# Kernel optimization log

Measured on AMD Instinct MI355X. Metric: run time of the kernel, lower is better.

Reference implementation:

```python
import jax, jax.numpy as jnp
import numpy as np

VOXEL_DIM = 16
CELL_DIM = 1.0
AA, A = 21, 14  # 20 amino acids + 'X'; atom14 representation
X_LBL = AA - 1  # label used for unknown residues


def make_voxel():
    v = VOXEL_DIM
    ax = jnp.arange(v, dtype=jnp.float32)
    vx = jnp.broadcast_to((ax - v / 2).reshape(-1, 1, 1), (v, v, v))
    vy = jnp.broadcast_to((ax - v / 4).reshape(1, -1, 1), (v, v, v))
    vz = jnp.broadcast_to((ax - v / 2).reshape(1, 1, -1), (v, v, v))
    return CELL_DIM * jnp.stack([vx, vy, vz], axis=3)  # (Vx,Vy,Vz,3)


def setup_inputs() -> dict:
    key = jax.random.key(0)
    k1, k2, k3, k4 = jax.random.split(key, 4)
    ZN = 1024
    C = 3.0 * jax.random.normal(k1, (ZN, A, 3), dtype=jnp.float32)
    L = jax.random.randint(k2, (ZN,), 0, AA)
    atom_mask = jnp.ones((ZN, A), dtype=jnp.float32)
    charges = 0.5 * jax.random.normal(k3, (AA, A), dtype=jnp.float32)
    return {"C": C, "L": L, "atom_mask": atom_mask, "charges": charges}


def get_backbone(C):
    n, ca, c = C[:, 0, :], C[:, 1, :], C[:, 2, :]
    b1 = ca - n
    b2 = c - ca
    b3 = jnp.cross(b1, b2)
    cb = ca - 0.58273431 * b2 + 0.56802827 * b1 - 0.54067466 * b3
    return jnp.stack([n, ca, c, cb], axis=1)  # (ZN,4,3)


def compute_frames(Cb):
    y = Cb[:, 3, :] - Cb[:, 1, :]
    y_unit = y / jnp.clip(jnp.linalg.norm(y, axis=1, keepdims=True), 1e-6)
    x_raw = Cb[:, 2, :] - Cb[:, 0, :]
    x_proj = jnp.sum(x_raw * y_unit, axis=1, keepdims=True)
    x = x_raw - x_proj
    x_unit = x / jnp.clip(jnp.linalg.norm(x, axis=1, keepdims=True), 1e-6)
    z = jnp.cross(x_unit, y_unit)
    z_unit = z / jnp.clip(jnp.linalg.norm(z, axis=1, keepdims=True), 1e-6)
    frames = jnp.stack([x_unit, y_unit, z_unit], axis=1)  # (ZN,3,3)
    return Cb[:, 3, :], frames


def compute_voxels(origins, frames, voxel):
    # rotation[n,x,y,z,s] = sum_u frames[n,u,s] * voxel[x,y,z,u]
    rot = jnp.einsum('nus,xyzu->nxyzs', frames, voxel)
    return origins[:, None, None, None, :] + rot  # (ZN,Vx,Vy,Vz,3)


def compute_fields(C, L, voxels, atom_mask, charges):
    L = jnp.where(L == -1, X_LBL, L)
    # (ZN,Vx,Vy,Vz,A,3)
    dv = voxels[:, :, :, :, None, :] - C[:, None, None, None, :, :]
    d = jnp.linalg.norm(dv, axis=-1, keepdims=True)
    dist_term = dv / (jnp.where(d == 0, 1.0, d) * jnp.clip(d, CELL_DIM) ** 2)
    pc = charges[L] * atom_mask  # (ZN,A)
    fields = jnp.einsum('na,nxyzas->nxyzs', pc, dist_term)
    fn = jnp.linalg.norm(fields, axis=-1, keepdims=True)
    fields = fields / jnp.where(fn == 0, 1.0, fn)
    return jnp.transpose(fields, (0, 4, 1, 2, 3))  # (ZN,3,Vx,Vy,Vz)


def compute_divergence(fields):
    r = CELL_DIM
    fx, fy, fz = fields[:, 0], fields[:, 1], fields[:, 2]
    dx = jnp.concatenate([
        ((fx[:, 1] - fx[:, 0]) / r)[:, None],
        (fx[:, 2:] - fx[:, :-2]) / (2 * r),
        ((fx[:, -1] - fx[:, -2]) / r)[:, None]], axis=1)
    dy = jnp.concatenate([
        ((fy[:, :, 1] - fy[:, :, 0]) / r)[:, :, None],
        (fy[:, :, 2:] - fy[:, :, :-2]) / (2 * r),
        ((fy[:, :, -1] - fy[:, :, -2]) / r)[:, :, None]], axis=2)
    dz = jnp.concatenate([
        ((fz[:, :, :, 1] - fz[:, :, :, 0]) / r)[:, :, :, None],
        (fz[:, :, :, 2:] - fz[:, :, :, :-2]) / (2 * r),
        ((fz[:, :, :, -1] - fz[:, :, :, -2]) / r)[:, :, :, None]], axis=3)
    return (dx + dy + dz)[:, None]  # (ZN,1,Vx,Vy,Vz)


def reference(C, L, atom_mask, charges):
    voxel = make_voxel()
    Cb = get_backbone(C)
    origins, frames = compute_frames(Cb)
    voxels = compute_voxels(origins, frames, voxel)
    fields = compute_fields(C, L, voxels, atom_mask, charges)
    div = compute_divergence(fields)
    return (Cb, div, frames)
```

## Files before the change

### kernel.cpp

```cpp
#include <hip/hip_runtime.h>
#include <hip/hip_bf16.h>

#define AA_NUM 21
#define A_NUM  14
#define NPTS   4096
#define BLK    512
#define PPT    (NPTS / BLK)

__device__ __forceinline__ float rfl(float x) {
    return __int_as_float(__builtin_amdgcn_readfirstlane(__float_as_int(x)));
}

__global__ __launch_bounds__(BLK) void preproc_kernel(
    const float* __restrict__ Cin,
    const int*   __restrict__ Lin,
    const float* __restrict__ Min,
    const float* __restrict__ Qin,
    float*       __restrict__ out,
    int ZN)
{
    __shared__ float s_atom[A_NUM][3];
    __shared__ float s_pc[A_NUM];
    __shared__ float s_fr[12];
    __shared__ float s_f[3][NPTS];

    const int n = blockIdx.x;
    const int t = threadIdx.x;
    const size_t div_off = (size_t)ZN * 12;
    const size_t fr_off  = div_off + (size_t)ZN * NPTS;

    if (t < A_NUM) {
        int la = Lin[n];
        la = (la == -1) ? (AA_NUM - 1) : la;
        float q = Qin[la * A_NUM + t];
        float m = Min[n * A_NUM + t];
        s_pc[t] = q * m;
        s_atom[t][0] = Cin[(n * A_NUM + t) * 3 + 0];
        s_atom[t][1] = Cin[(n * A_NUM + t) * 3 + 1];
        s_atom[t][2] = Cin[(n * A_NUM + t) * 3 + 2];
    }
    __syncthreads();

    if (t == 0) {
        const float c0 = 0.58273431f, c1 = 0.56802827f, c2 = 0.54067466f;
        float n0x = s_atom[0][0], n0y = s_atom[0][1], n0z = s_atom[0][2];
        float cax = s_atom[1][0], cay = s_atom[1][1], caz = s_atom[1][2];
        float ccx = s_atom[2][0], ccy = s_atom[2][1], ccz = s_atom[2][2];
        float b1x = cax - n0x, b1y = cay - n0y, b1z = caz - n0z;
        float b2x = ccx - cax, b2y = ccy - cay, b2z = ccz - caz;
        float b3x = b1y * b2z - b1z * b2y;
        float b3y = b1z * b2x - b1x * b2z;
        float b3z = b1x * b2y - b1y * b2x;
        float cbx = cax - c0 * b2x + c1 * b1x - c2 * b3x;
        float cby = cay - c0 * b2y + c1 * b1y - c2 * b3y;
        float cbz = caz - c0 * b2z + c1 * b1z - c2 * b3z;

        float* po = out + (size_t)n * 12;
        po[0]  = n0x; po[1]  = n0y; po[2]  = n0z;
        po[3]  = cax; po[4]  = cay; po[5]  = caz;
        po[6]  = ccx; po[7]  = ccy; po[8]  = ccz;
        po[9]  = cbx; po[10] = cby; po[11] = cbz;

        float yx = cbx - cax, yy = cby - cay, yz = cbz - caz;
        float yn = sqrtf(yx * yx + yy * yy + yz * yz);
        float yr = 1.0f / fmaxf(yn, 1e-6f);
        float yux = yx * yr, yuy = yy * yr, yuz = yz * yr;
        float xrx = ccx - n0x, xry = ccy - n0y, xrz = ccz - n0z;
        float xp = xrx * yux + xry * yuy + xrz * yuz;
        float xx = xrx - xp, xy = xry - xp, xz = xrz - xp;
        float xn = sqrtf(xx * xx + xy * xy + xz * xz);
        float xr = 1.0f / fmaxf(xn, 1e-6f);
        float xux = xx * xr, xuy = xy * xr, xuz = xz * xr;
        float zx = xuy * yuz - xuz * yuy;
        float zy = xuz * yux - xux * yuz;
        float zz = xux * yuy - xuy * yux;
        float zn = sqrtf(zx * zx + zy * zy + zz * zz);
        float zr = 1.0f / fmaxf(zn, 1e-6f);
        float zux = zx * zr, zuy = zy * zr, zuz = zz * zr;

        float* pf = out + fr_off + (size_t)n * 9;
        pf[0] = xux; pf[1] = xuy; pf[2] = xuz;
        pf[3] = yux; pf[4] = yuy; pf[5] = yuz;
        pf[6] = zux; pf[7] = zuy; pf[8] = zuz;

        s_fr[0] = xux; s_fr[1] = xuy; s_fr[2]  = xuz;
        s_fr[3] = yux; s_fr[4] = yuy; s_fr[5]  = yuz;
        s_fr[6] = zux; s_fr[7] = zuy; s_fr[8]  = zuz;
        s_fr[9] = cbx; s_fr[10] = cby; s_fr[11] = cbz;
    }
    __syncthreads();

    float ax[A_NUM], ay[A_NUM], az[A_NUM], aq[A_NUM];
    #pragma unroll
    for (int a = 0; a < A_NUM; ++a) {
        ax[a] = rfl(s_atom[a][0]);
        ay[a] = rfl(s_atom[a][1]);
        az[a] = rfl(s_atom[a][2]);
        aq[a] = rfl(s_pc[a]);
    }
    float fr[12];
    #pragma unroll
    for (int i = 0; i < 12; ++i) fr[i] = s_fr[i];

    #pragma unroll
    for (int k = 0; k < PPT; ++k) {
        int idx = t + k * BLK;
        float vx = (float)(idx >> 8) - 8.0f;
        float vy = (float)((idx >> 4) & 15) - 4.0f;
        float vz = (float)(idx & 15) - 8.0f;
        float px = fr[9]  + vx * fr[0] + vy * fr[3] + vz * fr[6];
        float py = fr[10] + vx * fr[1] + vy * fr[4] + vz * fr[7];
        float pz = fr[11] + vx * fr[2] + vy * fr[5] + vz * fr[8];
        float fx = 0.0f, fy = 0.0f, fz = 0.0f;
        #pragma unroll
        for (int a = 0; a < A_NUM; ++a) {
            float dx = px - ax[a], dy = py - ay[a], dz = pz - az[a];
            float d2 = dx * dx + dy * dy + dz * dz;
            float rq = __builtin_amdgcn_rsqf(d2);
            float mn = fminf(rq, 1.0f);
            float inv = rq * mn * mn;
            float w = (d2 != 0.0f) ? aq[a] * inv : 0.0f;
            fx = fmaf(w, dx, fx);
            fy = fmaf(w, dy, fy);
            fz = fmaf(w, dz, fz);
        }
        float fn2 = fx * fx + fy * fy + fz * fz;
        float rf = (fn2 != 0.0f) ? __builtin_amdgcn_rsqf(fn2) : 1.0f;
        s_f[0][idx] = fx * rf;
        s_f[1][idx] = fy * rf;
        s_f[2][idx] = fz * rf;
    }
    __syncthreads();

    float* dout = out + div_off + (size_t)n * NPTS;
    #pragma unroll
    for (int k = 0; k < PPT; ++k) {
        int idx = t + k * BLK;
        int xi = idx >> 8, yi = (idx >> 4) & 15, zi = idx & 15;
        int xm = xi - (xi > 0), xp = xi + (xi < 15);
        int ym = yi - (yi > 0), yp = yi + (yi < 15);
        int zm = zi - (zi > 0), zp = zi + (zi < 15);
        float sx = (xp - xm == 2) ? 0.5f : 1.0f;
        float sy = (yp - ym == 2) ? 0.5f : 1.0f;
        float sz = (zp - zm == 2) ? 0.5f : 1.0f;
        int byz = (yi << 4) | zi;
        int bxz = (xi << 8) | zi;
        int bxy = (xi << 8) | (yi << 4);
        float dxv = (s_f[0][(xp << 8) | byz] - s_f[0][(xm << 8) | byz]) * sx;
        float dyv = (s_f[1][bxz | (yp << 4)] - s_f[1][bxz | (ym << 4)]) * sy;
        float dzv = (s_f[2][bxy | zp]        - s_f[2][bxy | zm])        * sz;
        dout[idx] = dxv + dyv + dzv;
    }
}

extern "C" void kernel_launch(void* const* d_in, const int* in_sizes, int n_in,
                              void* d_out, int out_size, void* d_ws, size_t ws_size,
                              hipStream_t stream) {
    const float* C = (const float*)d_in[0];
    const int*   L = (const int*)d_in[1];
    const float* M = (const float*)d_in[2];
    const float* Q = (const float*)d_in[3];
    float* out = (float*)d_out;
    const int ZN = in_sizes[1];
    preproc_kernel<<<dim3(ZN), dim3(BLK), 0, stream>>>(C, L, M, Q, out, ZN);
}
```

Before: 92.63 us.

## Assign each thread a z-column so the z-derivative is computed in registers

Block size drops to 256, and each thread now computes all 16 z points of one (x,y) column. The z-component of the field stays in registers, so the z-derivative needs no shared memory and LDS use falls by a third. Each thread writes its divergence row with float4 stores, and the frame values are made wave-uniform with readfirstlane. In exchange, register pressure rises from the 16-element arrays, and each block has fewer threads to hide latency.

```diff
diff --git a/kernel.cpp b/kernel.cpp
--- a/kernel.cpp
+++ b/kernel.cpp
@@ -4,8 +4,7 @@
 #define AA_NUM 21
 #define A_NUM  14
 #define NPTS   4096
-#define BLK    512
-#define PPT    (NPTS / BLK)
+#define BLK    256
 
 __device__ __forceinline__ float rfl(float x) {
     return __int_as_float(__builtin_amdgcn_readfirstlane(__float_as_int(x)));
@@ -22,7 +21,8 @@
     __shared__ float s_atom[A_NUM][3];
     __shared__ float s_pc[A_NUM];
     __shared__ float s_fr[12];
-    __shared__ float s_f[3][NPTS];
+    __shared__ float s_fx[16][BLK];
+    __shared__ float s_fy[16][BLK];
 
     const int n = blockIdx.x;
     const int t = threadIdx.x;
@@ -32,9 +32,7 @@
     if (t < A_NUM) {
         int la = Lin[n];
         la = (la == -1) ? (AA_NUM - 1) : la;
-        float q = Qin[la * A_NUM + t];
-        float m = Min[n * A_NUM + t];
-        s_pc[t] = q * m;
+        s_pc[t] = Qin[la * A_NUM + t] * Min[n * A_NUM + t];
         s_atom[t][0] = Cin[(n * A_NUM + t) * 3 + 0];
         s_atom[t][1] = Cin[(n * A_NUM + t) * 3 + 1];
         s_atom[t][2] = Cin[(n * A_NUM + t) * 3 + 2];
@@ -62,20 +60,17 @@
         po[9]  = cbx; po[10] = cby; po[11] = cbz;
 
         float yx = cbx - cax, yy = cby - cay, yz = cbz - caz;
-        float yn = sqrtf(yx * yx + yy * yy + yz * yz);
-        float yr = 1.0f / fmaxf(yn, 1e-6f);
+        float yr = 1.0f / fmaxf(sqrtf(yx * yx + yy * yy + yz * yz), 1e-6f);
         float yux = yx * yr, yuy = yy * yr, yuz = yz * yr;
         float xrx = ccx - n0x, xry = ccy - n0y, xrz = ccz - n0z;
         float xp = xrx * yux + xry * yuy + xrz * yuz;
         float xx = xrx - xp, xy = xry - xp, xz = xrz - xp;
-        float xn = sqrtf(xx * xx + xy * xy + xz * xz);
-        float xr = 1.0f / fmaxf(xn, 1e-6f);
+        float xr = 1.0f / fmaxf(sqrtf(xx * xx + xy * xy + xz * xz), 1e-6f);
         float xux = xx * xr, xuy = xy * xr, xuz = xz * xr;
         float zx = xuy * yuz - xuz * yuy;
         float zy = xuz * yux - xux * yuz;
         float zz = xux * yuy - xuy * yux;
-        float zn = sqrtf(zx * zx + zy * zy + zz * zz);
-        float zr = 1.0f / fmaxf(zn, 1e-6f);
+        float zr = 1.0f / fmaxf(sqrtf(zx * zx + zy * zy + zz * zz), 1e-6f);
         float zux = zx * zr, zuy = zy * zr, zuz = zz * zr;
 
         float* pf = out + fr_off + (size_t)n * 9;
@@ -100,14 +95,18 @@
     }
     float fr[12];
     #pragma unroll
-    for (int i = 0; i < 12; ++i) fr[i] = s_fr[i];
+    for (int i = 0; i < 12; ++i) fr[i] = rfl(s_fr[i]);
+
+    const int xi = t >> 4;
+    const int yi = t & 15;
+    const float vx = (float)xi - 8.0f;
+    const float vy = (float)yi - 4.0f;
+
+    float fzv[16];
 
     #pragma unroll
-    for (int k = 0; k < PPT; ++k) {
-        int idx = t + k * BLK;
-        float vx = (float)(idx >> 8) - 8.0f;
-        float vy = (float)((idx >> 4) & 15) - 4.0f;
-        float vz = (float)(idx & 15) - 8.0f;
+    for (int z = 0; z < 16; ++z) {
+        float vz = (float)z - 8.0f;
         float px = fr[9]  + vx * fr[0] + vy * fr[3] + vz * fr[6];
         float py = fr[10] + vx * fr[1] + vy * fr[4] + vz * fr[7];
         float pz = fr[11] + vx * fr[2] + vy * fr[5] + vz * fr[8];
@@ -126,31 +125,34 @@
         }
         float fn2 = fx * fx + fy * fy + fz * fz;
         float rf = (fn2 != 0.0f) ? __builtin_amdgcn_rsqf(fn2) : 1.0f;
-        s_f[0][idx] = fx * rf;
-        s_f[1][idx] = fy * rf;
-        s_f[2][idx] = fz * rf;
+        s_fx[z][t] = fx * rf;
+        s_fy[z][t] = fy * rf;
+        fzv[z] = fz * rf;
     }
     __syncthreads();
 
-    float* dout = out + div_off + (size_t)n * NPTS;
+    const int cxp = t + ((xi < 15) ? 16 : 0);
+    const int cxm = t - ((xi > 0)  ? 16 : 0);
+    const int cyp = t + ((yi < 15) ? 1  : 0);
+    const int cym = t - ((yi > 0)  ? 1  : 0);
+    const float sx = (xi > 0 && xi < 15) ? 0.5f : 1.0f;
+    const float sy = (yi > 0 && yi < 15) ? 0.5f : 1.0f;
+
+    float dv[16];
     #pragma unroll
-    for (int k = 0; k < PPT; ++k) {
-        int idx = t + k * BLK;
-        int xi = idx >> 8, yi = (idx >> 4) & 15, zi = idx & 15;
-        int xm = xi - (xi > 0), xp = xi + (xi < 15);
-        int ym = yi - (yi > 0), yp = yi + (yi < 15);
-        int zm = zi - (zi > 0), zp = zi + (zi < 15);
-        float sx = (xp - xm == 2) ? 0.5f : 1.0f;
-        float sy = (yp - ym == 2) ? 0.5f : 1.0f;
-        float sz = (zp - zm == 2) ? 0.5f : 1.0f;
-        int byz = (yi << 4) | zi;
-        int bxz = (xi << 8) | zi;
-        int bxy = (xi << 8) | (yi << 4);
-        float dxv = (s_f[0][(xp << 8) | byz] - s_f[0][(xm << 8) | byz]) * sx;
-        float dyv = (s_f[1][bxz | (yp << 4)] - s_f[1][bxz | (ym << 4)]) * sy;
-        float dzv = (s_f[2][bxy | zp]        - s_f[2][bxy | zm])        * sz;
-        dout[idx] = dxv + dyv + dzv;
+    for (int z = 0; z < 16; ++z) {
+        int zp = z + (z < 15), zm = z - (z > 0);
+        float sz = (z > 0 && z < 15) ? 0.5f : 1.0f;
+        float dxv = (s_fx[z][cxp] - s_fx[z][cxm]) * sx;
+        float dyv = (s_fy[z][cyp] - s_fy[z][cym]) * sy;
+        float dzv = (fzv[zp] - fzv[zm]) * sz;
+        dv[z] = dxv + dyv + dzv;
     }
+
+    float4* dout = (float4*)(out + div_off + (size_t)n * NPTS + t * 16);
+    #pragma unroll
+    for (int q = 0; q < 4; ++q)
+        dout[q] = make_float4(dv[4 * q], dv[4 * q + 1], dv[4 * q + 2], dv[4 * q + 3]);
 }
 
 extern "C" void kernel_launch(void* const* d_in, const int* in_sizes, int n_in,
```

Result: slower. 101.9 us (+10.0%).
